# Performance work log

Measured on AMD Instinct MI355X. Metric: run time of the kernel, lower is better.

The kernel has to match this reference:

```python
import jax, jax.numpy as jnp
import numpy as np

CONF_THRESH = 0.25
IOU_THRESH = 0.45
MAX_PER_IMG = 100
K_PRE = 512          # fixed pre-NMS candidate count (padding for jit)
CLS_OFFSET = 4096.0  # class offset for non-class-agnostic NMS (torchvision batched_nms trick)


def setup_inputs() -> dict:
    key = jax.random.key(0)
    k1, k2, k3, k4 = jax.random.split(key, 4)
    B, N, C = 32, 8400, 80
    # YOLOX raw output layout: (cx, cy, w, h, obj, cls_0..cls_C-1)
    cxcy = jax.random.uniform(k1, (B, N, 2), dtype=jnp.float32) * 640.0
    wh = jax.random.uniform(k2, (B, N, 2), dtype=jnp.float32) * 128.0 + 4.0
    obj = jax.random.uniform(k3, (B, N, 1), dtype=jnp.float32)
    cls = jax.random.uniform(k4, (B, N, C), dtype=jnp.float32)
    pred = jnp.concatenate([cxcy, wh, obj, cls], axis=-1)  # [B, N, 85]
    return {"pred": pred}


def _pairwise_iou(b):
    # b: [K, 4] xyxy -> [K, K] IoU
    x1 = jnp.maximum(b[:, None, 0], b[None, :, 0])
    y1 = jnp.maximum(b[:, None, 1], b[None, :, 1])
    x2 = jnp.minimum(b[:, None, 2], b[None, :, 2])
    y2 = jnp.minimum(b[:, None, 3], b[None, :, 3])
    inter = jnp.clip(x2 - x1, 0.0) * jnp.clip(y2 - y1, 0.0)
    area = (b[:, 2] - b[:, 0]) * (b[:, 3] - b[:, 1])
    union = area[:, None] + area[None, :] - inter
    return inter / (union + 1e-9)


def _nms(boxes, valid):
    # boxes [K,4] already sorted by score desc; valid [K] bool. Greedy NMS.
    iou = _pairwise_iou(boxes)

    def body(i, keep):
        # keep[j] is False for j >= i, so this only checks earlier kept boxes
        suppressed = jnp.any(keep & (iou[i] > IOU_THRESH))
        return keep.at[i].set(valid[i] & jnp.logical_not(suppressed))

    return jax.lax.fori_loop(0, K_PRE, body, jnp.zeros(K_PRE, dtype=bool))


def reference(pred):
    # --- box decode: cxcywh -> xyxy (YOLOX postprocess box_corner) ---
    half = pred[..., 2:4] * 0.5
    boxes = jnp.concatenate([pred[..., :2] - half, pred[..., :2] + half], axis=-1)  # [B,N,4]
    obj = pred[..., 4]                 # [B,N]
    cls = pred[..., 5:]                # [B,N,C]
    class_conf = cls.max(axis=-1)      # [B,N]
    class_pred = jnp.argmax(cls, axis=-1)  # [B,N] int
    scores = obj * class_conf          # [B,N]

    # per-image adaptive conf: min(conf_thresh, best score) -> at least 1 survives
    conf = jnp.minimum(CONF_THRESH, scores.max(axis=-1, keepdims=True))  # [B,1]
    valid = scores >= conf
    masked = jnp.where(valid, scores, -jnp.inf)

    # fixed-size candidate set, sorted by score desc
    top_scores, idx = jax.lax.top_k(masked, K_PRE)  # [B,K]
    b_k = jnp.take_along_axis(boxes, idx[..., None], axis=1)       # [B,K,4]
    obj_k = jnp.take_along_axis(obj, idx, axis=1)                  # [B,K]
    cc_k = jnp.take_along_axis(class_conf, idx, axis=1)            # [B,K]
    cp_k = jnp.take_along_axis(class_pred, idx, axis=1)            # [B,K]
    valid_k = jnp.isfinite(top_scores)

    # class_agnostic=False: offset boxes by class so cross-class IoU is 0
    nms_boxes = b_k + cp_k.astype(b_k.dtype)[..., None] * CLS_OFFSET
    keep = jax.vmap(_nms)(nms_boxes, valid_k)  # [B,K] bool

    # compact kept boxes to the front (stable argsort preserves score order)
    order = jnp.argsort(jnp.where(keep, jnp.arange(K_PRE), K_PRE), axis=-1)
    sel = order[:, :MAX_PER_IMG]                                   # [B,M]
    mask = jnp.take_along_axis(keep, sel, axis=1)                  # [B,M]

    dets = jnp.concatenate(
        [b_k, obj_k[..., None], cc_k[..., None], cp_k.astype(b_k.dtype)[..., None]],
        axis=-1,
    )  # [B,K,7] = (x1,y1,x2,y2,obj,class_conf,class_pred)
    dets = jnp.take_along_axis(dets, sel[..., None], axis=1)       # [B,M,7]
    dets = dets * mask[..., None].astype(dets.dtype)
    return dets, mask
```

## Files before the change

kernel.cpp:

```cpp
#include <hip/hip_runtime.h>

#define NB 32
#define NN 8400
#define NC 80
#define KPRE 512
#define MAXOUT 100
#define NGRP 263
#define NWV 526

__global__ __launch_bounds__(128) void score_kernel(const float* __restrict__ pred,
                                                    float* __restrict__ scores,
                                                    unsigned* __restrict__ wmaxg,
                                                    float4* __restrict__ rawbox,
                                                    float4* __restrict__ minfo) {
    int b = blockIdx.y;
    int w = threadIdx.x >> 6, lane = threadIdx.x & 63;
    int g = blockIdx.x * 2 + w;
    __shared__ float4 stg4[2][340];
    const float4* p4 = (const float4*)pred;
    size_t base4 = (size_t)b * 178500 + (size_t)g * 340;
    size_t img_end4 = ((size_t)b + 1) * 178500;
    for (int k = lane; k < 340; k += 64) {
        size_t e = base4 + k;
        if (e >= img_end4) e = img_end4 - 1;
        stg4[w][k] = p4[e];
    }
    int rl = lane >> 2, q = lane & 3;
    int row = g * 16 + rl;
    const float* r = (const float*)&stg4[w][0] + rl * 85;
    float cx = r[0], cy = r[1], bw = r[2], bh = r[3], obj = r[4];
    int c0 = 5 + q * 20;
    float cc = r[c0];
    int cp = q * 20;
    for (int c = 1; c < 20; c++) {
        float v = r[c0 + c];
        if (v > cc) { cc = v; cp = q * 20 + c; }
    }
    {
        float cc1 = __shfl_xor(cc, 1, 64); int cp1 = __shfl_xor(cp, 1, 64);
        bool take = (cc1 > cc) || (cc1 == cc && cp1 < cp);
        cc = take ? cc1 : cc; cp = take ? cp1 : cp;
        float cc2 = __shfl_xor(cc, 2, 64); int cp2 = __shfl_xor(cp, 2, 64);
        take = (cc2 > cc) || (cc2 == cc && cp2 < cp);
        cc = take ? cc2 : cc; cp = take ? cp2 : cp;
    }
    float s = __fmul_rn(obj, cc);
    float hw = __fmul_rn(bw, 0.5f), hh = __fmul_rn(bh, 0.5f);
    float x1 = cx - hw, y1 = cy - hh, x2 = cx + hw, y2 = cy + hh;
    int srcl = (lane & 15) * 4;
    float v0 = __shfl(x1, srcl, 64);
    float v1 = __shfl(y1, srcl, 64);
    float v2 = __shfl(x2, srcl, 64);
    float v3 = __shfl(y2, srcl, 64);
    float v4 = __shfl(obj, srcl, 64);
    float v5 = __shfl(cc, srcl, 64);
    int   v6 = __shfl(cp, srcl, 64);
    float v7 = __shfl(s, srcl, 64);
    int wrow = g * 16 + (lane & 15);
    if (lane < 16 && wrow < NN) {
        size_t idx = (size_t)b * NN + wrow;
        scores[idx] = v7;
        rawbox[idx] = make_float4(v0, v1, v2, v3);
        minfo[idx]  = make_float4(v4, v5, (float)v6, v7);
    }
    if (row >= NN) s = 0.0f;
    unsigned bits = __float_as_uint(s);
    for (int o = 32; o > 0; o >>= 1) {
        unsigned other = (unsigned)__shfl_down((int)bits, o, 64);
        if (other > bits) bits = other;
    }
    if (lane == 0) wmaxg[b * NWV + g] = bits;
}

__device__ __forceinline__ void find_bin(const unsigned* hist, int cstart, unsigned T, int lane,
                                         int* outB, unsigned* outR) {
    unsigned running = 0;
    for (int c = cstart; c >= 0; c--) {
        unsigned v = hist[c * 64 + lane];
        unsigned s = v;
        for (int off = 1; off < 64; off <<= 1) {
            unsigned u = (unsigned)__shfl_down((int)s, off, 64);
            if (lane + off < 64) s += u;
        }
        unsigned total0 = (unsigned)__shfl((int)s, 0, 64);
        if (total0 + running >= T) {
            unsigned long long mask = __ballot(s + running >= T);
            int m = 63 - __clzll(mask);
            unsigned sm = (unsigned)__shfl((int)s, m, 64);
            unsigned vm = (unsigned)__shfl((int)v, m, 64);
            if (lane == 0) { *outB = c * 64 + m; *outR = T - (sm + running - vm); }
            return;
        }
        running += total0;
    }
    if (lane == 0) { *outB = 0; *outR = T; }
}

__global__ __launch_bounds__(1024) void selnms_kernel(const float* __restrict__ scores,
                                                      const unsigned* __restrict__ wmaxg,
                                                      const float4* __restrict__ rawbox,
                                                      const float4* __restrict__ minfo,
                                                      float* __restrict__ out) {
    int b = blockIdx.x, t = threadIdx.x;
    __shared__ unsigned histA[2048];
    __shared__ unsigned histB[2048];
    __shared__ unsigned long long list[KPRE];
    __shared__ unsigned long long sorted[KPRE];
    __shared__ unsigned long long elist64[256];
    __shared__ float4 sb[KPRE];
    __shared__ float4 sraw[KPRE];
    __shared__ float4 smeta[KPRE];
    __shared__ float  sarea[KPRE];
    __shared__ unsigned long long siou[KPRE * 8];
    __shared__ unsigned long long skeep[8];
    __shared__ int S_B[2];
    __shared__ unsigned S_T[2];
    __shared__ int S_cnt, S_ecnt, S_done;
    __shared__ float S_conf;
    __shared__ unsigned S_mbits;

    if (t == 0) { S_cnt = 0; S_ecnt = 0; }
    if (t < 64) {
        unsigned m = 0;
        for (int i = t; i < NWV; i += 64) {
            unsigned v = wmaxg[b * NWV + i];
            if (v > m) m = v;
        }
        for (int off = 32; off > 0; off >>= 1) {
            unsigned o = (unsigned)__shfl_down((int)m, off, 64);
            if (o > m) m = o;
        }
        if (t == 0) { S_conf = fminf(0.25f, __uint_as_float(m)); S_mbits = m; }
    }
    for (int i = t; i < 2048; i += 1024) { histA[i] = 0; histB[i] = 0; }
    for (int i = t; i < KPRE * 8; i += 1024) siou[i] = 0ull;
    __syncthreads();
    float conf = S_conf;
    const float4* sc4 = (const float4*)(scores + (size_t)b * NN);
    unsigned ka[8];
    unsigned kb[4] = {0u, 0u, 0u, 0u};
    {
        float4 u0 = sc4[2 * t], u1 = sc4[2 * t + 1];
        ka[0] = (u0.x >= conf) ? __float_as_uint(u0.x) : 0u;
        ka[1] = (u0.y >= conf) ? __float_as_uint(u0.y) : 0u;
        ka[2] = (u0.z >= conf) ? __float_as_uint(u0.z) : 0u;
        ka[3] = (u0.w >= conf) ? __float_as_uint(u0.w) : 0u;
        ka[4] = (u1.x >= conf) ? __float_as_uint(u1.x) : 0u;
        ka[5] = (u1.y >= conf) ? __float_as_uint(u1.y) : 0u;
        ka[6] = (u1.z >= conf) ? __float_as_uint(u1.z) : 0u;
        ka[7] = (u1.w >= conf) ? __float_as_uint(u1.w) : 0u;
        if (t < 52) {
            float4 u2 = sc4[2048 + t];
            kb[0] = (u2.x >= conf) ? __float_as_uint(u2.x) : 0u;
            kb[1] = (u2.y >= conf) ? __float_as_uint(u2.y) : 0u;
            kb[2] = (u2.z >= conf) ? __float_as_uint(u2.z) : 0u;
            kb[3] = (u2.w >= conf) ? __float_as_uint(u2.w) : 0u;
        }
#pragma unroll
        for (int j = 0; j < 8; j++) atomicAdd(&histA[ka[j] >> 21], 1u);
        if (t < 52) {
#pragma unroll
            for (int j = 0; j < 4; j++) atomicAdd(&histA[kb[j] >> 21], 1u);
        }
    }
    __syncthreads();
    if (t < 64) {
        int cs = (int)(S_mbits >> 27); if (cs > 31) cs = 31;
        find_bin(histA, cs, 512u, t, &S_B[0], &S_T[0]);
    }
    __syncthreads();
    int B1 = S_B[0]; unsigned R1 = S_T[0];
#pragma unroll
    for (int j = 0; j < 8; j++) {
        unsigned k = ka[j];
        if ((int)(k >> 21) == B1) atomicAdd(&histB[(k >> 10) & 0x7FFu], 1u);
    }
    if (t < 52) {
#pragma unroll
        for (int j = 0; j < 4; j++) {
            unsigned k = kb[j];
            if ((int)(k >> 21) == B1) atomicAdd(&histB[(k >> 10) & 0x7FFu], 1u);
        }
    }
    __syncthreads();
    if (t < 64) find_bin(histB, 31, R1, t, &S_B[1], &S_T[1]);
    __syncthreads();
    unsigned P = ((unsigned)B1 << 11) | (unsigned)S_B[1];
    unsigned R2 = S_T[1];
#pragma unroll
    for (int j = 0; j < 8; j++) {
        unsigned k = ka[j];
        unsigned n = 8u * (unsigned)t + (unsigned)j;
        if ((k >> 10) > P) {
            int pos = atomicAdd(&S_cnt, 1);
            list[pos] = ((unsigned long long)k << 32) | (unsigned long long)(unsigned)(~n);
        } else if (P != 0u && (k >> 10) == P) {
            int ep = atomicAdd(&S_ecnt, 1);
            if (ep < 256) elist64[ep] = ((unsigned long long)k << 32) | (unsigned long long)(unsigned)(~n);
        }
    }
    if (t < 52) {
#pragma unroll
        for (int j = 0; j < 4; j++) {
            unsigned k = kb[j];
            unsigned n = 8192u + 4u * (unsigned)t + (unsigned)j;
            if ((k >> 10) > P) {
                int pos = atomicAdd(&S_cnt, 1);
                list[pos] = ((unsigned long long)k << 32) | (unsigned long long)(unsigned)(~n);
            } else if (P != 0u && (k >> 10) == P) {
                int ep = atomicAdd(&S_ecnt, 1);
                if (ep < 256) elist64[ep] = ((unsigned long long)k << 32) | (unsigned long long)(unsigned)(~n);
            }
        }
    }
    __syncthreads();
    int ecnt = S_ecnt; if (ecnt > 256) ecnt = 256;
    if (t < ecnt) {
        unsigned long long my = elist64[t];
        int r = 0;
        for (int j = 0; j < ecnt; j++) r += (elist64[j] > my) ? 1 : 0;
        if (r < (int)R2) {
            int pos = atomicAdd(&S_cnt, 1);
            list[pos] = my;
        }
    }
    __syncthreads();
    int nval = S_cnt;
    for (int i = nval + t; i < KPRE; i += 1024) list[i] = 0ull;
    __syncthreads();
    if (t < KPRE) {
        unsigned long long K0 = list[t];
        int r0 = 0;
        for (int j = 0; j < KPRE; j++) {
            unsigned long long L = list[j];
            r0 += (L > K0) ? 1 : 0;
        }
        if (K0 != 0ull) sorted[r0] = K0; else sorted[t] = 0ull;
    }
    __syncthreads();
    if (t < KPRE) {
        unsigned long long key = sorted[t];
        int valid = ((unsigned)(key >> 32)) != 0u;
        unsigned n = ~(unsigned)key;
        if (!valid) n = 0;
        size_t src = (size_t)b * NN + n;
        float4 rb = rawbox[src];
        float4 mi = minfo[src];
        float off = __fmul_rn(mi.z, 4096.0f);
        float4 bo = make_float4(rb.x + off, rb.y + off, rb.z + off, rb.w + off);
        sraw[t] = rb;
        sb[t] = bo;
        smeta[t] = make_float4(mi.x, mi.y, mi.z, valid ? 1.0f : 0.0f);
        sarea[t] = __fmul_rn(bo.z - bo.x, bo.w - bo.y);
    }
    __syncthreads();

    unsigned long long keepW = 0ull;
    int cnt = 0;
    int lg = t >> 3, lw = t & 7;
    int irow = t >> 4, iq = t & 15;

    for (int c = 0; c < 8; c++) {
        int row = (c << 6) + irow;
        float4 bi = sb[row];
        float ai = sarea[row];
        for (int k = 0; k <= c; k++) {
            unsigned long long wk = 0ull;
            int j0 = (k << 6) + iq;
#pragma unroll
            for (int s = 0; s < 4; s++) {
                int j = j0 + (s << 4);
                float4 bj = sb[j];
                float xx1 = fmaxf(bi.x, bj.x);
                float yy1 = fmaxf(bi.y, bj.y);
                float xx2 = fminf(bi.z, bj.z);
                float yy2 = fminf(bi.w, bj.w);
                float iw = fmaxf(xx2 - xx1, 0.0f);
                float ih = fmaxf(yy2 - yy1, 0.0f);
                float inter = __fmul_rn(iw, ih);
                float uni = (ai + sarea[j]) - inter;
                float iou = inter / (uni + 1e-9f);
                if (iou > 0.45f && j < row) wk |= 1ull << (j & 63);
            }
            if (wk) atomicOr(&siou[(row << 3) + k], wk);
        }
        __syncthreads();
        if (t < 64) {
            unsigned long long R[8];
#pragma unroll
            for (int k = 0; k < 8; k++) R[k] = siou[(c << 9) + (k << 6) + t];
#pragma unroll
            for (int k = 0; k < 8; k++) {
#pragma unroll
                for (int m = 0; m < 8; m++) {
                    int ii = (c << 6) + (k << 3) + m;
                    bool hit = (lg == m) && ((R[k] & keepW) != 0ull);
                    unsigned long long bal = __ballot(hit);
                    bool kept = (bal == 0ull) && (ii < nval);
                    if (kept) {
                        cnt++;
                        if (lw == c) keepW |= 1ull << ((k << 3) + m);
                    }
                }
            }
            if (t == 0) S_done = (cnt >= MAXOUT) ? 1 : 0;
        }
        __syncthreads();
        if (S_done) break;
    }
    if (t < 8) skeep[t] = keepW;
    __syncthreads();

    float* dets = out + (size_t)b * (MAXOUT * 7);
    float* maskp = out + (size_t)NB * MAXOUT * 7 + (size_t)b * MAXOUT;
    for (int m = t; m < MAXOUT * 7; m += 1024) dets[m] = 0.0f;
    for (int m = t; m < MAXOUT; m += 1024) maskp[m] = 0.0f;
    __syncthreads();
    if (t < KPRE) {
        int wq = t >> 6;
        unsigned long long kw = skeep[wq];
        if ((kw >> (t & 63)) & 1ull) {
            int rank = __popcll(kw & ((1ull << (t & 63)) - 1ull));
            for (int w2 = 0; w2 < wq; w2++) rank += __popcll(skeep[w2]);
            if (rank < MAXOUT) {
                float4 rb = sraw[t];
                float4 mt = smeta[t];
                float* rowp = dets + rank * 7;
                rowp[0] = rb.x; rowp[1] = rb.y; rowp[2] = rb.z; rowp[3] = rb.w;
                rowp[4] = mt.x; rowp[5] = mt.y; rowp[6] = mt.z;
                maskp[rank] = 1.0f;
            }
        }
    }
}

extern "C" void kernel_launch(void* const* d_in, const int* in_sizes, int n_in,
                              void* d_out, int out_size, void* d_ws, size_t ws_size,
                              hipStream_t stream) {
    const float* pred = (const float*)d_in[0];
    float* out = (float*)d_out;

    char* ws = (char*)d_ws;
    unsigned* wmaxg = (unsigned*)ws;
    float* scores = (float*)(ws + 67584);
    float4* rawbox = (float4*)(ws + 1142784);
    float4* minfo  = (float4*)(ws + 5443584);

    dim3 gA(NGRP, NB);
    score_kernel<<<gA, 128, 0, stream>>>(pred, scores, wmaxg, rawbox, minfo);
    selnms_kernel<<<NB, 1024, 0, stream>>>(scores, wmaxg, rawbox, minfo, out);
}
```

Before: 170.1 us.

## Fuse score and NMS kernels via cooperative grid sync, drop box/meta buffers

The two kernels are merged into one cooperative launch with a grid-wide sync, with a two-kernel fallback if the cooperative launch fails. The score pass now writes only scores and per-wave maxima and no longer stores decoded boxes, metadata or argmax. The NMS stage re-reads the 512 selected rows from pred and recomputes the decode and class argmax. The rank sort is split across both halves of the block with vectorized compares, and find_bin prefetches the next histogram row. This cuts global write traffic and one launch, at the cost of grid-sync overhead, a serial 80-class scan per selected candidate, and only 32 of 256 blocks active after the sync.

```diff
diff --git a/kernel.cpp b/kernel.cpp
--- a/kernel.cpp
+++ b/kernel.cpp
@@ -1,82 +1,88 @@
 #include <hip/hip_runtime.h>
+#include <hip/hip_cooperative_groups.h>
+
+namespace cg = cooperative_groups;
 
 #define NB 32
 #define NN 8400
 #define NC 80
 #define KPRE 512
 #define MAXOUT 100
-#define NGRP 263
 #define NWV 526
-
-__global__ __launch_bounds__(128) void score_kernel(const float* __restrict__ pred,
-                                                    float* __restrict__ scores,
-                                                    unsigned* __restrict__ wmaxg,
-                                                    float4* __restrict__ rawbox,
-                                                    float4* __restrict__ minfo) {
-    int b = blockIdx.y;
-    int w = threadIdx.x >> 6, lane = threadIdx.x & 63;
-    int g = blockIdx.x * 2 + w;
-    __shared__ float4 stg4[2][340];
-    const float4* p4 = (const float4*)pred;
+#define NGROUPS (NB * NWV)
+#define GRID1 256
+
+struct P2 {
+    unsigned histA[2048];
+    unsigned histB[2048];
+    unsigned long long list[KPRE];
+    unsigned long long sorted[KPRE];
+    unsigned long long elist64[256];
+    int srank[KPRE];
+    float4 sb[KPRE];
+    float4 sraw[KPRE];
+    float4 smeta[KPRE];
+    float sarea[KPRE];
+    unsigned long long siou[KPRE * 8];
+    unsigned long long skeep[8];
+    int S_B[2];
+    unsigned S_T[2];
+    int S_cnt, S_ecnt, S_done;
+    float S_conf;
+    unsigned S_mbits;
+};
+
+union __align__(16) SMem {
+    float4 stg[16][340];
+    P2 p2;
+};
+
+__device__ __forceinline__ void score_group(const float4* __restrict__ p4, int gg, int w, int lane,
+                                            float4 (*stg)[340],
+                                            float* __restrict__ scores,
+                                            unsigned* __restrict__ wmaxg) {
+    int b = gg / NWV, g = gg - b * NWV;
     size_t base4 = (size_t)b * 178500 + (size_t)g * 340;
     size_t img_end4 = ((size_t)b + 1) * 178500;
     for (int k = lane; k < 340; k += 64) {
         size_t e = base4 + k;
         if (e >= img_end4) e = img_end4 - 1;
-        stg4[w][k] = p4[e];
+        stg[w][k] = p4[e];
     }
     int rl = lane >> 2, q = lane & 3;
     int row = g * 16 + rl;
-    const float* r = (const float*)&stg4[w][0] + rl * 85;
-    float cx = r[0], cy = r[1], bw = r[2], bh = r[3], obj = r[4];
+    const float* r = (const float*)&stg[w][0] + rl * 85;
+    float obj = r[4];
     int c0 = 5 + q * 20;
     float cc = r[c0];
-    int cp = q * 20;
     for (int c = 1; c < 20; c++) {
         float v = r[c0 + c];
-        if (v > cc) { cc = v; cp = q * 20 + c; }
+        if (v > cc) cc = v;
     }
     {
-        float cc1 = __shfl_xor(cc, 1, 64); int cp1 = __shfl_xor(cp, 1, 64);
-        bool take = (cc1 > cc) || (cc1 == cc && cp1 < cp);
-        cc = take ? cc1 : cc; cp = take ? cp1 : cp;
-        float cc2 = __shfl_xor(cc, 2, 64); int cp2 = __shfl_xor(cp, 2, 64);
-        take = (cc2 > cc) || (cc2 == cc && cp2 < cp);
-        cc = take ? cc2 : cc; cp = take ? cp2 : cp;
+        float cc1 = __shfl_xor(cc, 1, 64); if (cc1 > cc) cc = cc1;
+        float cc2 = __shfl_xor(cc, 2, 64); if (cc2 > cc) cc = cc2;
     }
     float s = __fmul_rn(obj, cc);
-    float hw = __fmul_rn(bw, 0.5f), hh = __fmul_rn(bh, 0.5f);
-    float x1 = cx - hw, y1 = cy - hh, x2 = cx + hw, y2 = cy + hh;
     int srcl = (lane & 15) * 4;
-    float v0 = __shfl(x1, srcl, 64);
-    float v1 = __shfl(y1, srcl, 64);
-    float v2 = __shfl(x2, srcl, 64);
-    float v3 = __shfl(y2, srcl, 64);
-    float v4 = __shfl(obj, srcl, 64);
-    float v5 = __shfl(cc, srcl, 64);
-    int   v6 = __shfl(cp, srcl, 64);
     float v7 = __shfl(s, srcl, 64);
     int wrow = g * 16 + (lane & 15);
-    if (lane < 16 && wrow < NN) {
-        size_t idx = (size_t)b * NN + wrow;
-        scores[idx] = v7;
-        rawbox[idx] = make_float4(v0, v1, v2, v3);
-        minfo[idx]  = make_float4(v4, v5, (float)v6, v7);
-    }
+    if (lane < 16 && wrow < NN) scores[(size_t)b * NN + wrow] = v7;
     if (row >= NN) s = 0.0f;
     unsigned bits = __float_as_uint(s);
     for (int o = 32; o > 0; o >>= 1) {
         unsigned other = (unsigned)__shfl_down((int)bits, o, 64);
         if (other > bits) bits = other;
     }
-    if (lane == 0) wmaxg[b * NWV + g] = bits;
+    if (lane == 0) wmaxg[gg] = bits;
 }
 
 __device__ __forceinline__ void find_bin(const unsigned* hist, int cstart, unsigned T, int lane,
                                          int* outB, unsigned* outR) {
     unsigned running = 0;
+    unsigned v = hist[cstart * 64 + lane];
     for (int c = cstart; c >= 0; c--) {
-        unsigned v = hist[c * 64 + lane];
+        unsigned vn = (c > 0) ? hist[(c - 1) * 64 + lane] : 0u;
         unsigned s = v;
         for (int off = 1; off < 64; off <<= 1) {
             unsigned u = (unsigned)__shfl_down((int)s, off, 64);
@@ -92,50 +98,38 @@
             return;
         }
         running += total0;
+        v = vn;
     }
     if (lane == 0) { *outB = 0; *outR = T; }
 }
 
-__global__ __launch_bounds__(1024) void selnms_kernel(const float* __restrict__ scores,
-                                                      const unsigned* __restrict__ wmaxg,
-                                                      const float4* __restrict__ rawbox,
-                                                      const float4* __restrict__ minfo,
-                                                      float* __restrict__ out) {
-    int b = blockIdx.x, t = threadIdx.x;
-    __shared__ unsigned histA[2048];
-    __shared__ unsigned histB[2048];
-    __shared__ unsigned long long list[KPRE];
-    __shared__ unsigned long long sorted[KPRE];
-    __shared__ unsigned long long elist64[256];
-    __shared__ float4 sb[KPRE];
-    __shared__ float4 sraw[KPRE];
-    __shared__ float4 smeta[KPRE];
-    __shared__ float  sarea[KPRE];
-    __shared__ unsigned long long siou[KPRE * 8];
-    __shared__ unsigned long long skeep[8];
-    __shared__ int S_B[2];
-    __shared__ unsigned S_T[2];
-    __shared__ int S_cnt, S_ecnt, S_done;
-    __shared__ float S_conf;
-    __shared__ unsigned S_mbits;
-
-    if (t == 0) { S_cnt = 0; S_ecnt = 0; }
+__device__ __forceinline__ void selnms_body(P2& S, int b, int t,
+                                            const float* __restrict__ pred,
+                                            const float* __restrict__ scores,
+                                            const unsigned* __restrict__ wmaxg,
+                                            float* __restrict__ out) {
+    if (t == 0) { S.S_cnt = 0; S.S_ecnt = 0; S.S_done = 0; }
     if (t < 64) {
+        unsigned tmp[9];
+#pragma unroll
+        for (int k = 0; k < 9; k++) {
+            int i = t + k * 64;
+            tmp[k] = (i < NWV) ? wmaxg[b * NWV + i] : 0u;
+        }
         unsigned m = 0;
-        for (int i = t; i < NWV; i += 64) {
-            unsigned v = wmaxg[b * NWV + i];
-            if (v > m) m = v;
-        }
+#pragma unroll
+        for (int k = 0; k < 9; k++) if (tmp[k] > m) m = tmp[k];
         for (int off = 32; off > 0; off >>= 1) {
             unsigned o = (unsigned)__shfl_down((int)m, off, 64);
             if (o > m) m = o;
         }
-        if (t == 0) { S_conf = fminf(0.25f, __uint_as_float(m)); S_mbits = m; }
-    }
-    for (int i = t; i < 2048; i += 1024) { histA[i] = 0; histB[i] = 0; }
-    for (int i = t; i < KPRE * 8; i += 1024) siou[i] = 0ull;
-    __syncthreads();
-    float conf = S_conf;
+        if (t == 0) { S.S_conf = fminf(0.25f, __uint_as_float(m)); S.S_mbits = m; }
+    }
+    for (int i = t; i < 2048; i += 1024) { S.histA[i] = 0; S.histB[i] = 0; }
+    for (int i = t; i < KPRE * 8; i += 1024) S.siou[i] = 0ull;
+    if (t < 256) S.elist64[t] = 0ull;
+    __syncthreads();
+    float conf = S.S_conf;
     const float4* sc4 = (const float4*)(scores + (size_t)b * NN);
     unsigned ka[8];
     unsigned kb[4] = {0u, 0u, 0u, 0u};
@@ -157,46 +151,46 @@
             kb[3] = (u2.w >= conf) ? __float_as_uint(u2.w) : 0u;
         }
 #pragma unroll
-        for (int j = 0; j < 8; j++) atomicAdd(&histA[ka[j] >> 21], 1u);
+        for (int j = 0; j < 8; j++) atomicAdd(&S.histA[ka[j] >> 21], 1u);
         if (t < 52) {
 #pragma unroll
-            for (int j = 0; j < 4; j++) atomicAdd(&histA[kb[j] >> 21], 1u);
+            for (int j = 0; j < 4; j++) atomicAdd(&S.histA[kb[j] >> 21], 1u);
         }
     }
     __syncthreads();
     if (t < 64) {
-        int cs = (int)(S_mbits >> 27); if (cs > 31) cs = 31;
-        find_bin(histA, cs, 512u, t, &S_B[0], &S_T[0]);
-    }
-    __syncthreads();
-    int B1 = S_B[0]; unsigned R1 = S_T[0];
+        int cs = (int)(S.S_mbits >> 27); if (cs > 31) cs = 31;
+        find_bin(S.histA, cs, 512u, t, &S.S_B[0], &S.S_T[0]);
+    }
+    __syncthreads();
+    int B1 = S.S_B[0]; unsigned R1 = S.S_T[0];
 #pragma unroll
     for (int j = 0; j < 8; j++) {
         unsigned k = ka[j];
-        if ((int)(k >> 21) == B1) atomicAdd(&histB[(k >> 10) & 0x7FFu], 1u);
+        if ((int)(k >> 21) == B1) atomicAdd(&S.histB[(k >> 10) & 0x7FFu], 1u);
     }
     if (t < 52) {
 #pragma unroll
         for (int j = 0; j < 4; j++) {
             unsigned k = kb[j];
-            if ((int)(k >> 21) == B1) atomicAdd(&histB[(k >> 10) & 0x7FFu], 1u);
-        }
-    }
-    __syncthreads();
-    if (t < 64) find_bin(histB, 31, R1, t, &S_B[1], &S_T[1]);
-    __syncthreads();
-    unsigned P = ((unsigned)B1 << 11) | (unsigned)S_B[1];
-    unsigned R2 = S_T[1];
+            if ((int)(k >> 21) == B1) atomicAdd(&S.histB[(k >> 10) & 0x7FFu], 1u);
+        }
+    }
+    __syncthreads();
+    if (t < 64) find_bin(S.histB, 31, R1, t, &S.S_B[1], &S.S_T[1]);
+    __syncthreads();
+    unsigned P = ((unsigned)B1 << 11) | (unsigned)S.S_B[1];
+    unsigned R2 = S.S_T[1];
 #pragma unroll
     for (int j = 0; j < 8; j++) {
         unsigned k = ka[j];
         unsigned n = 8u * (unsigned)t + (unsigned)j;
         if ((k >> 10) > P) {
-            int pos = atomicAdd(&S_cnt, 1);
-            list[pos] = ((unsigned long long)k << 32) | (unsigned long long)(unsigned)(~n);
+            int pos = atomicAdd(&S.S_cnt, 1);
+            S.list[pos] = ((unsigned long long)k << 32) | (unsigned long long)(unsigned)(~n);
         } else if (P != 0u && (k >> 10) == P) {
-            int ep = atomicAdd(&S_ecnt, 1);
-            if (ep < 256) elist64[ep] = ((unsigned long long)k << 32) | (unsigned long long)(unsigned)(~n);
+            int ep = atomicAdd(&S.S_ecnt, 1);
+            if (ep < 256) S.elist64[ep] = ((unsigned long long)k << 32) | (unsigned long long)(unsigned)(~n);
         }
     }
     if (t < 52) {
@@ -205,53 +199,75 @@
             unsigned k = kb[j];
             unsigned n = 8192u + 4u * (unsigned)t + (unsigned)j;
             if ((k >> 10) > P) {
-                int pos = atomicAdd(&S_cnt, 1);
-                list[pos] = ((unsigned long long)k << 32) | (unsigned long long)(unsigned)(~n);
+                int pos = atomicAdd(&S.S_cnt, 1);
+                S.list[pos] = ((unsigned long long)k << 32) | (unsigned long long)(unsigned)(~n);
             } else if (P != 0u && (k >> 10) == P) {
-                int ep = atomicAdd(&S_ecnt, 1);
-                if (ep < 256) elist64[ep] = ((unsigned long long)k << 32) | (unsigned long long)(unsigned)(~n);
+                int ep = atomicAdd(&S.S_ecnt, 1);
+                if (ep < 256) S.elist64[ep] = ((unsigned long long)k << 32) | (unsigned long long)(unsigned)(~n);
             }
         }
     }
     __syncthreads();
-    int ecnt = S_ecnt; if (ecnt > 256) ecnt = 256;
+    int ecnt = S.S_ecnt; if (ecnt > 256) ecnt = 256;
     if (t < ecnt) {
-        unsigned long long my = elist64[t];
+        unsigned long long my = S.elist64[t];
+        const ulonglong2* e2 = (const ulonglong2*)S.elist64;
         int r = 0;
-        for (int j = 0; j < ecnt; j++) r += (elist64[j] > my) ? 1 : 0;
+#pragma unroll 4
+        for (int j = 0; j < 128; j += 4) {
+            ulonglong2 a = e2[j], b2 = e2[j + 1], c2 = e2[j + 2], d2 = e2[j + 3];
+            r += (int)(a.x > my) + (int)(a.y > my) + (int)(b2.x > my) + (int)(b2.y > my);
+            r += (int)(c2.x > my) + (int)(c2.y > my) + (int)(d2.x > my) + (int)(d2.y > my);
+        }
         if (r < (int)R2) {
-            int pos = atomicAdd(&S_cnt, 1);
-            list[pos] = my;
-        }
-    }
-    __syncthreads();
-    int nval = S_cnt;
-    for (int i = nval + t; i < KPRE; i += 1024) list[i] = 0ull;
+            int pos = atomicAdd(&S.S_cnt, 1);
+            S.list[pos] = my;
+        }
+    }
+    __syncthreads();
+    int nval = S.S_cnt;
+    for (int i = nval + t; i < KPRE; i += 1024) S.list[i] = 0ull;
+    __syncthreads();
+    {
+        int tt = t & 511, half = t >> 9;
+        unsigned long long K0 = S.list[tt];
+        const ulonglong2* l2 = (const ulonglong2*)S.list;
+        int jb = half * 128;
+        int r0 = 0;
+#pragma unroll 4
+        for (int j = 0; j < 128; j += 4) {
+            ulonglong2 a = l2[jb + j], b2 = l2[jb + j + 1], c2 = l2[jb + j + 2], d2 = l2[jb + j + 3];
+            r0 += (int)(a.x > K0) + (int)(a.y > K0) + (int)(b2.x > K0) + (int)(b2.y > K0);
+            r0 += (int)(c2.x > K0) + (int)(c2.y > K0) + (int)(d2.x > K0) + (int)(d2.y > K0);
+        }
+        if (half) S.srank[tt] = r0;
+        __syncthreads();
+        if (!half) {
+            int r = r0 + S.srank[tt];
+            if (K0 != 0ull) S.sorted[r] = K0; else S.sorted[tt] = 0ull;
+        }
+    }
     __syncthreads();
     if (t < KPRE) {
-        unsigned long long K0 = list[t];
-        int r0 = 0;
-        for (int j = 0; j < KPRE; j++) {
-            unsigned long long L = list[j];
-            r0 += (L > K0) ? 1 : 0;
-        }
-        if (K0 != 0ull) sorted[r0] = K0; else sorted[t] = 0ull;
-    }
-    __syncthreads();
-    if (t < KPRE) {
-        unsigned long long key = sorted[t];
+        unsigned long long key = S.sorted[t];
         int valid = ((unsigned)(key >> 32)) != 0u;
         unsigned n = ~(unsigned)key;
         if (!valid) n = 0;
-        size_t src = (size_t)b * NN + n;
-        float4 rb = rawbox[src];
-        float4 mi = minfo[src];
-        float off = __fmul_rn(mi.z, 4096.0f);
-        float4 bo = make_float4(rb.x + off, rb.y + off, rb.z + off, rb.w + off);
-        sraw[t] = rb;
-        sb[t] = bo;
-        smeta[t] = make_float4(mi.x, mi.y, mi.z, valid ? 1.0f : 0.0f);
-        sarea[t] = __fmul_rn(bo.z - bo.x, bo.w - bo.y);
+        const float* pr = pred + ((size_t)b * NN + n) * 85;
+        float cx = pr[0], cy = pr[1], bw = pr[2], bh = pr[3], obj = pr[4];
+        float cc = pr[5]; int cp = 0;
+        for (int c = 1; c < NC; c++) {
+            float v = pr[5 + c];
+            if (v > cc) { cc = v; cp = c; }
+        }
+        float hw = __fmul_rn(bw, 0.5f), hh = __fmul_rn(bh, 0.5f);
+        float x1 = cx - hw, y1 = cy - hh, x2 = cx + hw, y2 = cy + hh;
+        float off = __fmul_rn((float)cp, 4096.0f);
+        float4 bo = make_float4(x1 + off, y1 + off, x2 + off, y2 + off);
+        S.sraw[t] = make_float4(x1, y1, x2, y2);
+        S.sb[t] = bo;
+        S.smeta[t] = make_float4(obj, cc, (float)cp, valid ? 1.0f : 0.0f);
+        S.sarea[t] = __fmul_rn(bo.z - bo.x, bo.w - bo.y);
     }
     __syncthreads();
 
@@ -262,15 +278,15 @@
 
     for (int c = 0; c < 8; c++) {
         int row = (c << 6) + irow;
-        float4 bi = sb[row];
-        float ai = sarea[row];
+        float4 bi = S.sb[row];
+        float ai = S.sarea[row];
         for (int k = 0; k <= c; k++) {
             unsigned long long wk = 0ull;
             int j0 = (k << 6) + iq;
 #pragma unroll
             for (int s = 0; s < 4; s++) {
                 int j = j0 + (s << 4);
-                float4 bj = sb[j];
+                float4 bj = S.sb[j];
                 float xx1 = fmaxf(bi.x, bj.x);
                 float yy1 = fmaxf(bi.y, bj.y);
                 float xx2 = fminf(bi.z, bj.z);
@@ -278,17 +294,17 @@
                 float iw = fmaxf(xx2 - xx1, 0.0f);
                 float ih = fmaxf(yy2 - yy1, 0.0f);
                 float inter = __fmul_rn(iw, ih);
-                float uni = (ai + sarea[j]) - inter;
+                float uni = (ai + S.sarea[j]) - inter;
                 float iou = inter / (uni + 1e-9f);
                 if (iou > 0.45f && j < row) wk |= 1ull << (j & 63);
             }
-            if (wk) atomicOr(&siou[(row << 3) + k], wk);
+            if (wk) atomicOr(&S.siou[(row << 3) + k], wk);
         }
         __syncthreads();
         if (t < 64) {
             unsigned long long R[8];
 #pragma unroll
-            for (int k = 0; k < 8; k++) R[k] = siou[(c << 9) + (k << 6) + t];
+            for (int k = 0; k < 8; k++) R[k] = S.siou[(c << 9) + (k << 6) + t];
 #pragma unroll
             for (int k = 0; k < 8; k++) {
 #pragma unroll
@@ -303,12 +319,12 @@
                     }
                 }
             }
-            if (t == 0) S_done = (cnt >= MAXOUT) ? 1 : 0;
+            if (t == 0) S.S_done = (cnt >= MAXOUT) ? 1 : 0;
         }
         __syncthreads();
-        if (S_done) break;
-    }
-    if (t < 8) skeep[t] = keepW;
+        if (S.S_done) break;
+    }
+    if (t < 8) S.skeep[t] = keepW;
     __syncthreads();
 
     float* dets = out + (size_t)b * (MAXOUT * 7);
@@ -318,13 +334,13 @@
     __syncthreads();
     if (t < KPRE) {
         int wq = t >> 6;
-        unsigned long long kw = skeep[wq];
+        unsigned long long kw = S.skeep[wq];
         if ((kw >> (t & 63)) & 1ull) {
             int rank = __popcll(kw & ((1ull << (t & 63)) - 1ull));
-            for (int w2 = 0; w2 < wq; w2++) rank += __popcll(skeep[w2]);
+            for (int w2 = 0; w2 < wq; w2++) rank += __popcll(S.skeep[w2]);
             if (rank < MAXOUT) {
-                float4 rb = sraw[t];
-                float4 mt = smeta[t];
+                float4 rb = S.sraw[t];
+                float4 mt = S.smeta[t];
                 float* rowp = dets + rank * 7;
                 rowp[0] = rb.x; rowp[1] = rb.y; rowp[2] = rb.z; rowp[3] = rb.w;
                 rowp[4] = mt.x; rowp[5] = mt.y; rowp[6] = mt.z;
@@ -334,6 +350,44 @@
     }
 }
 
+__global__ __launch_bounds__(1024) void fused_kernel(const float* __restrict__ pred,
+                                                     float* __restrict__ scores,
+                                                     unsigned* __restrict__ wmaxg,
+                                                     float* __restrict__ out) {
+    __shared__ SMem sm;
+    int t = threadIdx.x;
+    int w = t >> 6, lane = t & 63;
+    int wid = blockIdx.x * 16 + w;
+    int nw = gridDim.x * 16;
+    const float4* p4 = (const float4*)pred;
+    for (int gg = wid; gg < NGROUPS; gg += nw)
+        score_group(p4, gg, w, lane, sm.stg, scores, wmaxg);
+    cg::this_grid().sync();
+    if (blockIdx.x < NB)
+        selnms_body(sm.p2, blockIdx.x, t, pred, scores, wmaxg, out);
+}
+
+__global__ __launch_bounds__(1024) void score2_kernel(const float* __restrict__ pred,
+                                                      float* __restrict__ scores,
+                                                      unsigned* __restrict__ wmaxg) {
+    __shared__ SMem sm;
+    int t = threadIdx.x;
+    int w = t >> 6, lane = t & 63;
+    int wid = blockIdx.x * 16 + w;
+    int nw = gridDim.x * 16;
+    const float4* p4 = (const float4*)pred;
+    for (int gg = wid; gg < NGROUPS; gg += nw)
+        score_group(p4, gg, w, lane, sm.stg, scores, wmaxg);
+}
+
+__global__ __launch_bounds__(1024) void selnms2_kernel(const float* __restrict__ pred,
+                                                       const float* __restrict__ scores,
+                                                       const unsigned* __restrict__ wmaxg,
+                                                       float* __restrict__ out) {
+    __shared__ SMem sm;
+    selnms_body(sm.p2, blockIdx.x, threadIdx.x, pred, scores, wmaxg, out);
+}
+
 extern "C" void kernel_launch(void* const* d_in, const int* in_sizes, int n_in,
                               void* d_out, int out_size, void* d_ws, size_t ws_size,
                               hipStream_t stream) {
@@ -343,10 +397,13 @@
     char* ws = (char*)d_ws;
     unsigned* wmaxg = (unsigned*)ws;
     float* scores = (float*)(ws + 67584);
-    float4* rawbox = (float4*)(ws + 1142784);
-    float4* minfo  = (float4*)(ws + 5443584);
-
-    dim3 gA(NGRP, NB);
-    score_kernel<<<gA, 128, 0, stream>>>(pred, scores, wmaxg, rawbox, minfo);
-    selnms_kernel<<<NB, 1024, 0, stream>>>(scores, wmaxg, rawbox, minfo, out);
-}
+
+    void* args[4] = { (void*)&pred, (void*)&scores, (void*)&wmaxg, (void*)&out };
+    hipError_t err = hipLaunchCooperativeKernel(fused_kernel, dim3(GRID1), dim3(1024),
+                                                args, 0, stream);
+    if (err != hipSuccess) {
+        (void)hipGetLastError();
+        score2_kernel<<<256, 1024, 0, stream>>>(pred, scores, wmaxg);
+        selnms2_kernel<<<NB, 1024, 0, stream>>>(pred, scores, wmaxg, out);
+    }
+}
```

New measurement: 216.2 us. 1.27x slower.

## Aggregate wave atomics, split rank sort across all threads, vectorise LDS scans

Applied to the files above, without the earlier changes.

Replaces per-element shared atomics in candidate compaction with wave-level ballot/popcount aggregation. The 512-key rank sort now uses all 1024 threads, each half counting over half the list, with the partial ranks combined through shared memory. The tie-list rank loop runs a fixed 256 entries using 128-bit LDS loads, which is why elist64 is now zero-initialised. find_bin prefetches the next histogram row, and the wmax reduction is unrolled. These target serialised LDS atomics and long sequential scans in the selection phase, at the cost of an extra barrier and fixed-length loops.

```diff
diff --git a/kernel.cpp b/kernel.cpp
--- a/kernel.cpp
+++ b/kernel.cpp
@@ -75,8 +75,9 @@
 __device__ __forceinline__ void find_bin(const unsigned* hist, int cstart, unsigned T, int lane,
                                          int* outB, unsigned* outR) {
     unsigned running = 0;
+    unsigned v = hist[cstart * 64 + lane];
     for (int c = cstart; c >= 0; c--) {
-        unsigned v = hist[c * 64 + lane];
+        unsigned vn = (c > 0) ? hist[(c - 1) * 64 + lane] : 0u;
         unsigned s = v;
         for (int off = 1; off < 64; off <<= 1) {
             unsigned u = (unsigned)__shfl_down((int)s, off, 64);
@@ -92,6 +93,7 @@
             return;
         }
         running += total0;
+        v = vn;
     }
     if (lane == 0) { *outB = 0; *outR = T; }
 }
@@ -102,11 +104,13 @@
                                                       const float4* __restrict__ minfo,
                                                       float* __restrict__ out) {
     int b = blockIdx.x, t = threadIdx.x;
+    int lane = t & 63;
     __shared__ unsigned histA[2048];
     __shared__ unsigned histB[2048];
     __shared__ unsigned long long list[KPRE];
     __shared__ unsigned long long sorted[KPRE];
     __shared__ unsigned long long elist64[256];
+    __shared__ int srank[KPRE];
     __shared__ float4 sb[KPRE];
     __shared__ float4 sraw[KPRE];
     __shared__ float4 smeta[KPRE];
@@ -119,13 +123,17 @@
     __shared__ float S_conf;
     __shared__ unsigned S_mbits;
 
-    if (t == 0) { S_cnt = 0; S_ecnt = 0; }
+    if (t == 0) { S_cnt = 0; S_ecnt = 0; S_done = 0; }
     if (t < 64) {
+        unsigned tmp[9];
+#pragma unroll
+        for (int k = 0; k < 9; k++) {
+            int i = t + k * 64;
+            tmp[k] = (i < NWV) ? wmaxg[b * NWV + i] : 0u;
+        }
         unsigned m = 0;
-        for (int i = t; i < NWV; i += 64) {
-            unsigned v = wmaxg[b * NWV + i];
-            if (v > m) m = v;
-        }
+#pragma unroll
+        for (int k = 0; k < 9; k++) if (tmp[k] > m) m = tmp[k];
         for (int off = 32; off > 0; off >>= 1) {
             unsigned o = (unsigned)__shfl_down((int)m, off, 64);
             if (o > m) m = o;
@@ -134,6 +142,7 @@
     }
     for (int i = t; i < 2048; i += 1024) { histA[i] = 0; histB[i] = 0; }
     for (int i = t; i < KPRE * 8; i += 1024) siou[i] = 0ull;
+    if (t < 256) elist64[t] = 0ull;
     __syncthreads();
     float conf = S_conf;
     const float4* sc4 = (const float4*)(scores + (size_t)b * NN);
@@ -187,16 +196,28 @@
     __syncthreads();
     unsigned P = ((unsigned)B1 << 11) | (unsigned)S_B[1];
     unsigned R2 = S_T[1];
+    unsigned long long ltmask = (1ull << lane) - 1ull;
 #pragma unroll
     for (int j = 0; j < 8; j++) {
         unsigned k = ka[j];
         unsigned n = 8u * (unsigned)t + (unsigned)j;
-        if ((k >> 10) > P) {
-            int pos = atomicAdd(&S_cnt, 1);
-            list[pos] = ((unsigned long long)k << 32) | (unsigned long long)(unsigned)(~n);
-        } else if (P != 0u && (k >> 10) == P) {
-            int ep = atomicAdd(&S_ecnt, 1);
-            if (ep < 256) elist64[ep] = ((unsigned long long)k << 32) | (unsigned long long)(unsigned)(~n);
+        unsigned long long key = ((unsigned long long)k << 32) | (unsigned long long)(unsigned)(~n);
+        bool win = (k >> 10) > P;
+        bool tie = (P != 0u) && ((k >> 10) == P);
+        unsigned long long mw = __ballot(win);
+        unsigned long long mtie = __ballot(tie);
+        int baseW = 0, baseT = 0;
+        if (lane == 0) {
+            if (mw)   baseW = atomicAdd(&S_cnt, __popcll(mw));
+            if (mtie) baseT = atomicAdd(&S_ecnt, __popcll(mtie));
+        }
+        baseW = __shfl(baseW, 0, 64);
+        baseT = __shfl(baseT, 0, 64);
+        if (win) {
+            list[baseW + __popcll(mw & ltmask)] = key;
+        } else if (tie) {
+            int ep = baseT + __popcll(mtie & ltmask);
+            if (ep < 256) elist64[ep] = key;
         }
     }
     if (t < 52) {
@@ -204,12 +225,23 @@
         for (int j = 0; j < 4; j++) {
             unsigned k = kb[j];
             unsigned n = 8192u + 4u * (unsigned)t + (unsigned)j;
-            if ((k >> 10) > P) {
-                int pos = atomicAdd(&S_cnt, 1);
-                list[pos] = ((unsigned long long)k << 32) | (unsigned long long)(unsigned)(~n);
-            } else if (P != 0u && (k >> 10) == P) {
-                int ep = atomicAdd(&S_ecnt, 1);
-                if (ep < 256) elist64[ep] = ((unsigned long long)k << 32) | (unsigned long long)(unsigned)(~n);
+            unsigned long long key = ((unsigned long long)k << 32) | (unsigned long long)(unsigned)(~n);
+            bool win = (k >> 10) > P;
+            bool tie = (P != 0u) && ((k >> 10) == P);
+            unsigned long long mw = __ballot(win);
+            unsigned long long mtie = __ballot(tie);
+            int baseW = 0, baseT = 0;
+            if (lane == 0) {
+                if (mw)   baseW = atomicAdd(&S_cnt, __popcll(mw));
+                if (mtie) baseT = atomicAdd(&S_ecnt, __popcll(mtie));
+            }
+            baseW = __shfl(baseW, 0, 64);
+            baseT = __shfl(baseT, 0, 64);
+            if (win) {
+                list[baseW + __popcll(mw & ltmask)] = key;
+            } else if (tie) {
+                int ep = baseT + __popcll(mtie & ltmask);
+                if (ep < 256) elist64[ep] = key;
             }
         }
     }
@@ -217,8 +249,14 @@
     int ecnt = S_ecnt; if (ecnt > 256) ecnt = 256;
     if (t < ecnt) {
         unsigned long long my = elist64[t];
+        const ulonglong2* e2 = (const ulonglong2*)elist64;
         int r = 0;
-        for (int j = 0; j < ecnt; j++) r += (elist64[j] > my) ? 1 : 0;
+#pragma unroll 4
+        for (int j = 0; j < 128; j += 4) {
+            ulonglong2 a = e2[j], b2 = e2[j + 1], c2 = e2[j + 2], d2 = e2[j + 3];
+            r += (int)(a.x > my) + (int)(a.y > my) + (int)(b2.x > my) + (int)(b2.y > my);
+            r += (int)(c2.x > my) + (int)(c2.y > my) + (int)(d2.x > my) + (int)(d2.y > my);
+        }
         if (r < (int)R2) {
             int pos = atomicAdd(&S_cnt, 1);
             list[pos] = my;
@@ -228,14 +266,24 @@
     int nval = S_cnt;
     for (int i = nval + t; i < KPRE; i += 1024) list[i] = 0ull;
     __syncthreads();
-    if (t < KPRE) {
-        unsigned long long K0 = list[t];
+    {
+        int tt = t & 511, half = t >> 9;
+        unsigned long long K0 = list[tt];
+        const ulonglong2* l2 = (const ulonglong2*)list;
+        int jb = half * 128;
         int r0 = 0;
-        for (int j = 0; j < KPRE; j++) {
-            unsigned long long L = list[j];
-            r0 += (L > K0) ? 1 : 0;
-        }
-        if (K0 != 0ull) sorted[r0] = K0; else sorted[t] = 0ull;
+#pragma unroll 4
+        for (int j = 0; j < 128; j += 4) {
+            ulonglong2 a = l2[jb + j], b2 = l2[jb + j + 1], c2 = l2[jb + j + 2], d2 = l2[jb + j + 3];
+            r0 += (int)(a.x > K0) + (int)(a.y > K0) + (int)(b2.x > K0) + (int)(b2.y > K0);
+            r0 += (int)(c2.x > K0) + (int)(c2.y > K0) + (int)(d2.x > K0) + (int)(d2.y > K0);
+        }
+        if (half) srank[tt] = r0;
+        __syncthreads();
+        if (!half) {
+            int r = r0 + srank[tt];
+            if (K0 != 0ull) sorted[r] = K0; else sorted[tt] = 0ull;
+        }
     }
     __syncthreads();
     if (t < KPRE) {
```

Measured after the change: 167.6 us. No clear change (-1.4%).
